# Kernel tuning notes

Measured on AMD Instinct MI355X. Metric: run time of the kernel, lower is better.

The kernel has to match this reference:

```python
import jax, jax.numpy as jnp
import numpy as np

BLOCKSIZE = 64
# Fixed NF4 codebook (bitsandbytes normal-float 4-bit quantiles)
NF4_CODE = jnp.array([
    -1.0, -0.6961928009986877, -0.5250730514526367, -0.39491748809814453,
    -0.28444138169288635, -0.18477343022823334, -0.09105003625154495, 0.0,
    0.07958029955625534, 0.16093020141124725, 0.24611230194568634,
    0.33791524171829224, 0.44070982933044434, 0.5626170039176941,
    0.7229568362236023, 1.0], dtype=jnp.float32)


def setup_inputs() -> dict:
    key = jax.random.key(0)
    k1, k2, k3, k4 = jax.random.split(key, 4)
    B, IN, OUT = 32, 4096, 14336
    x = jax.random.normal(k1, (B, IN), dtype=jnp.float32)
    codes = jax.random.randint(k2, (OUT, IN), 0, 16, dtype=jnp.int32)
    absmax = jax.random.uniform(k3, (OUT * IN // BLOCKSIZE,), dtype=jnp.float32)
    bias = jax.random.normal(k4, (OUT,), dtype=jnp.float32)
    return {"x": x, "codes": codes, "absmax": absmax, "bias": bias}


def reference(x, codes, absmax, bias):
    out_f, in_f = codes.shape
    # Dequantize: codebook lookup then per-block (64) absmax scaling
    w = NF4_CODE[codes].reshape(-1, BLOCKSIZE) * absmax[:, None]  # [nblocks, 64]
    w = w.reshape(out_f, in_f)
    # y = x @ W^T + bias  (matmul_4bit semantics)
    return jnp.einsum('bi,oi->bo', x, w) + bias
```

## Files before the change

kernel.cpp:

```cpp
#include <hip/hip_runtime.h>
#include <stddef.h>
#include <stdint.h>

#define B_     32
#define IN_    4096
#define OUT_   14336
#define KSPLIT 8
#define KRANGE (IN_ / KSPLIT)
#define NSTEP  (KRANGE / 32)
#define POUT   (B_ * OUT_)

typedef _Float16 v2h __attribute__((ext_vector_type(2)));
typedef _Float16 v8h __attribute__((ext_vector_type(8)));
typedef float    v4f __attribute__((ext_vector_type(4)));
typedef int      v4i __attribute__((ext_vector_type(4)));

__device__ __constant__ float c_nf4[16] = {
    -1.0f, -0.6961928009986877f, -0.5250730514526367f, -0.39491748809814453f,
    -0.28444138169288635f, -0.18477343022823334f, -0.09105003625154495f, 0.0f,
    0.07958029955625534f, 0.16093020141124725f, 0.24611230194568634f,
    0.33791524171829224f, 0.44070982933044434f, 0.5626170039176941f,
    0.7229568362236023f, 1.0f};

__global__ __launch_bounds__(256) void prep(const float* __restrict__ x,
                                            unsigned* __restrict__ xB) {
    int t  = blockIdx.x * 256 + threadIdx.x;
    int kt = t >> 7;
    int bt = (t >> 6) & 1;
    int l  = t & 63;
    int b  = bt * 16 + (l & 15);
    int k0 = kt * 32 + (l >> 4) * 8;
    const float* xr = x + (size_t)b * IN_ + k0;
    float4 a = *(const float4*)xr;
    float4 c = *(const float4*)(xr + 4);
    union { v2h h; unsigned u; } p0, p1, p2, p3;
    p0.h = (v2h){(_Float16)a.x, (_Float16)a.y};
    p1.h = (v2h){(_Float16)a.z, (_Float16)a.w};
    p2.h = (v2h){(_Float16)c.x, (_Float16)c.y};
    p3.h = (v2h){(_Float16)c.z, (_Float16)c.w};
    uint4 w = {p0.u, p1.u, p2.u, p3.u};
    *(uint4*)(xB + (size_t)t * 4) = w;
}

__global__ __launch_bounds__(256) void init_out(const float* __restrict__ bias,
                                                float* __restrict__ out) {
    int i4 = (blockIdx.x * 256 + threadIdx.x) * 4;
    int o = i4 % OUT_;
    *(float4*)(out + i4) = *(const float4*)(bias + o);
}

__global__ __launch_bounds__(256) void reduce_out(const float* __restrict__ partial,
                                                  const float* __restrict__ bias,
                                                  float* __restrict__ out) {
    int i4 = (blockIdx.x * 256 + threadIdx.x) * 4;
    int o = i4 % OUT_;
    float4 r = *(const float4*)(bias + o);
#pragma unroll
    for (int s = 0; s < KSPLIT; ++s) {
        float4 p = *(const float4*)(partial + (size_t)s * POUT + i4);
        r.x += p.x; r.y += p.y; r.z += p.z; r.w += p.w;
    }
    *(float4*)(out + i4) = r;
}

#define ROWSTRIDE 67

template <int ATOMIC>
__global__ __launch_bounds__(256) void nf4_mfma(
    const int* __restrict__ codes, const float* __restrict__ absmax,
    const unsigned* __restrict__ xB, float* __restrict__ dst) {
    __shared__ unsigned stage[4 * 16 * ROWSTRIDE];
    __shared__ v2h lut2[256];

    const int tid = threadIdx.x;
    {
        float lo = c_nf4[tid & 15], hi = c_nf4[tid >> 4];
        lut2[tid] = (v2h){(_Float16)lo, (_Float16)hi};
    }
    __syncthreads();

    const int w  = tid >> 6;
    const int l  = tid & 63;
    const int ot = blockIdx.x >> 3;
    const int ks = blockIdx.x & 7;
    const int m  = l & 15;
    const int q  = l >> 4;
    const int o0 = ot * 64 + w * 16;

    unsigned* sw = stage + w * 16 * ROWSTRIDE;

#pragma unroll 4
    for (int i = 0; i < 16; ++i) {
        const v4i* rp = (const v4i*)(codes + (size_t)(o0 + i) * IN_ + ks * KRANGE);
        v4i a0 = __builtin_nontemporal_load(rp + 2 * l);
        v4i a1 = __builtin_nontemporal_load(rp + 2 * l + 1);
        unsigned pk = (unsigned)(a0[0] | (a0[1] << 4)) |
                      ((unsigned)(a0[2] | (a0[3] << 4)) << 8) |
                      ((unsigned)(a1[0] | (a1[1] << 4)) << 16) |
                      ((unsigned)(a1[2] | (a1[3] << 4)) << 24);
        sw[i * ROWSTRIDE + l] = pk;
    }

    const float* amrow = absmax + (size_t)(o0 + m) * 64 + ks * (KRANGE / 64);
    const uint4* xbp   = (const uint4*)xB + (size_t)(ks * NSTEP) * 128 + l;

    v4f acc0 = {0.f, 0.f, 0.f, 0.f};
    v4f acc1 = {0.f, 0.f, 0.f, 0.f};

#pragma unroll 4
    for (int kt = 0; kt < NSTEP; ++kt) {
        unsigned pk = sw[m * ROWSTRIDE + kt * 4 + q];
        uint4 b0 = xbp[(size_t)kt * 128];
        uint4 b1 = xbp[(size_t)kt * 128 + 64];
        float amf = amrow[kt >> 1];
        _Float16 ah = (_Float16)amf;
        v2h amh = (v2h){ah, ah};

        union { v2h h[4]; v8h v; } A;
        A.h[0] = lut2[pk & 255] * amh;
        A.h[1] = lut2[(pk >> 8) & 255] * amh;
        A.h[2] = lut2[(pk >> 16) & 255] * amh;
        A.h[3] = lut2[pk >> 24] * amh;

        union { uint4 u; v8h v; } F0, F1;
        F0.u = b0;
        F1.u = b1;
        acc0 = __builtin_amdgcn_mfma_f32_16x16x32_f16(A.v, F0.v, acc0, 0, 0, 0);
        acc1 = __builtin_amdgcn_mfma_f32_16x16x32_f16(A.v, F1.v, acc1, 0, 0, 0);
    }

    const int bc = l & 15;
    const int ob = o0 + q * 4;
#pragma unroll
    for (int r = 0; r < 4; ++r) {
        if (ATOMIC) {
            atomicAdd(dst + (size_t)bc * OUT_ + ob + r, acc0[r]);
            atomicAdd(dst + (size_t)(bc + 16) * OUT_ + ob + r, acc1[r]);
        } else {
            dst[((size_t)ks * B_ + bc) * OUT_ + ob + r]      = acc0[r];
            dst[((size_t)ks * B_ + bc + 16) * OUT_ + ob + r] = acc1[r];
        }
    }
}

extern "C" void kernel_launch(void* const* d_in, const int* in_sizes, int n_in,
                              void* d_out, int out_size, void* d_ws, size_t ws_size,
                              hipStream_t stream) {
    const float* x      = (const float*)d_in[0];
    const int*   codes  = (const int*)d_in[1];
    const float* absmax = (const float*)d_in[2];
    const float* bias   = (const float*)d_in[3];
    float* out = (float*)d_out;
    unsigned* xB = (unsigned*)d_ws;

    prep<<<dim3(64), 256, 0, stream>>>(x, xB);

    const size_t need = 262144 + (size_t)KSPLIT * POUT * 4;
    if (ws_size >= need) {
        float* partial = (float*)((char*)d_ws + 262144);
        nf4_mfma<0><<<dim3(224 * KSPLIT), 256, 0, stream>>>(codes, absmax, xB, partial);
        reduce_out<<<dim3(POUT / 1024), 256, 0, stream>>>(partial, bias, out);
    } else {
        init_out<<<dim3(POUT / 1024), 256, 0, stream>>>(bias, out);
        nf4_mfma<1><<<dim3(224 * KSPLIT), 256, 0, stream>>>(codes, absmax, xB, out);
    }
}
```

Before: 330.6 us.

## Drop split-K and fuse bias into single-pass NF4 MFMA kernel

Removes the K-split across blocks, so each block now loops over all eight K sections for its 64 output rows. Bias is added in the kernel epilogue, which eliminates the partial-sum buffer, the reduce kernel and the atomic fallback path. Code loads for each section are fully unrolled, and absmax values are fetched as vectors. The grid shrinks from 1792 to 224 blocks, which is fewer than the CU count. That cuts parallelism and latency hiding for a kernel dominated by streaming the int32 codes.

```diff
diff --git a/kernel.cpp b/kernel.cpp
--- a/kernel.cpp
+++ b/kernel.cpp
@@ -2,13 +2,12 @@
 #include <stddef.h>
 #include <stdint.h>
 
-#define B_     32
-#define IN_    4096
-#define OUT_   14336
-#define KSPLIT 8
-#define KRANGE (IN_ / KSPLIT)
-#define NSTEP  (KRANGE / 32)
-#define POUT   (B_ * OUT_)
+#define B_   32
+#define IN_  4096
+#define OUT_ 14336
+#define NSEC 8
+#define SECK 512
+#define ROWSTRIDE 67
 
 typedef _Float16 v2h __attribute__((ext_vector_type(2)));
 typedef _Float16 v8h __attribute__((ext_vector_type(8)));
@@ -42,33 +41,10 @@
     *(uint4*)(xB + (size_t)t * 4) = w;
 }
 
-__global__ __launch_bounds__(256) void init_out(const float* __restrict__ bias,
-                                                float* __restrict__ out) {
-    int i4 = (blockIdx.x * 256 + threadIdx.x) * 4;
-    int o = i4 % OUT_;
-    *(float4*)(out + i4) = *(const float4*)(bias + o);
-}
-
-__global__ __launch_bounds__(256) void reduce_out(const float* __restrict__ partial,
-                                                  const float* __restrict__ bias,
-                                                  float* __restrict__ out) {
-    int i4 = (blockIdx.x * 256 + threadIdx.x) * 4;
-    int o = i4 % OUT_;
-    float4 r = *(const float4*)(bias + o);
-#pragma unroll
-    for (int s = 0; s < KSPLIT; ++s) {
-        float4 p = *(const float4*)(partial + (size_t)s * POUT + i4);
-        r.x += p.x; r.y += p.y; r.z += p.z; r.w += p.w;
-    }
-    *(float4*)(out + i4) = r;
-}
-
-#define ROWSTRIDE 67
-
-template <int ATOMIC>
 __global__ __launch_bounds__(256) void nf4_mfma(
     const int* __restrict__ codes, const float* __restrict__ absmax,
-    const unsigned* __restrict__ xB, float* __restrict__ dst) {
+    const unsigned* __restrict__ xB, const float* __restrict__ bias,
+    float* __restrict__ out) {
     __shared__ unsigned stage[4 * 16 * ROWSTRIDE];
     __shared__ v2h lut2[256];
 
@@ -81,65 +57,65 @@
 
     const int w  = tid >> 6;
     const int l  = tid & 63;
-    const int ot = blockIdx.x >> 3;
-    const int ks = blockIdx.x & 7;
     const int m  = l & 15;
     const int q  = l >> 4;
-    const int o0 = ot * 64 + w * 16;
+    const int o0 = blockIdx.x * 64 + w * 16;
 
     unsigned* sw = stage + w * 16 * ROWSTRIDE;
-
-#pragma unroll 4
-    for (int i = 0; i < 16; ++i) {
-        const v4i* rp = (const v4i*)(codes + (size_t)(o0 + i) * IN_ + ks * KRANGE);
-        v4i a0 = __builtin_nontemporal_load(rp + 2 * l);
-        v4i a1 = __builtin_nontemporal_load(rp + 2 * l + 1);
-        unsigned pk = (unsigned)(a0[0] | (a0[1] << 4)) |
-                      ((unsigned)(a0[2] | (a0[3] << 4)) << 8) |
-                      ((unsigned)(a1[0] | (a1[1] << 4)) << 16) |
-                      ((unsigned)(a1[2] | (a1[3] << 4)) << 24);
-        sw[i * ROWSTRIDE + l] = pk;
-    }
-
-    const float* amrow = absmax + (size_t)(o0 + m) * 64 + ks * (KRANGE / 64);
-    const uint4* xbp   = (const uint4*)xB + (size_t)(ks * NSTEP) * 128 + l;
+    const float* amrow = absmax + (size_t)(o0 + m) * 64;
+    const uint4* xbp   = (const uint4*)xB + l;
 
     v4f acc0 = {0.f, 0.f, 0.f, 0.f};
     v4f acc1 = {0.f, 0.f, 0.f, 0.f};
 
-#pragma unroll 4
-    for (int kt = 0; kt < NSTEP; ++kt) {
-        unsigned pk = sw[m * ROWSTRIDE + kt * 4 + q];
-        uint4 b0 = xbp[(size_t)kt * 128];
-        uint4 b1 = xbp[(size_t)kt * 128 + 64];
-        float amf = amrow[kt >> 1];
-        _Float16 ah = (_Float16)amf;
-        v2h amh = (v2h){ah, ah};
+#pragma unroll 1
+    for (int s = 0; s < NSEC; ++s) {
+#pragma unroll
+        for (int i = 0; i < 16; ++i) {
+            const v4i* rp = (const v4i*)(codes + (size_t)(o0 + i) * IN_ + s * SECK);
+            v4i a0 = __builtin_nontemporal_load(rp + 2 * l);
+            v4i a1 = __builtin_nontemporal_load(rp + 2 * l + 1);
+            unsigned pk = (unsigned)(a0[0] | (a0[1] << 4)) |
+                          ((unsigned)(a0[2] | (a0[3] << 4)) << 8) |
+                          ((unsigned)(a1[0] | (a1[1] << 4)) << 16) |
+                          ((unsigned)(a1[2] | (a1[3] << 4)) << 24);
+            sw[i * ROWSTRIDE + l] = pk;
+        }
 
-        union { v2h h[4]; v8h v; } A;
-        A.h[0] = lut2[pk & 255] * amh;
-        A.h[1] = lut2[(pk >> 8) & 255] * amh;
-        A.h[2] = lut2[(pk >> 16) & 255] * amh;
-        A.h[3] = lut2[pk >> 24] * amh;
+        float4 amlo = *(const float4*)(amrow + s * 8);
+        float4 amhi = *(const float4*)(amrow + s * 8 + 4);
+        const float ams[8] = {amlo.x, amlo.y, amlo.z, amlo.w,
+                              amhi.x, amhi.y, amhi.z, amhi.w};
 
-        union { uint4 u; v8h v; } F0, F1;
-        F0.u = b0;
-        F1.u = b1;
-        acc0 = __builtin_amdgcn_mfma_f32_16x16x32_f16(A.v, F0.v, acc0, 0, 0, 0);
-        acc1 = __builtin_amdgcn_mfma_f32_16x16x32_f16(A.v, F1.v, acc1, 0, 0, 0);
+#pragma unroll
+        for (int kt = 0; kt < 16; ++kt) {
+            unsigned pk = sw[m * ROWSTRIDE + kt * 4 + q];
+            uint4 b0 = xbp[(size_t)(s * 16 + kt) * 128];
+            uint4 b1 = xbp[(size_t)(s * 16 + kt) * 128 + 64];
+            _Float16 ah = (_Float16)ams[kt >> 1];
+            v2h amh = (v2h){ah, ah};
+
+            union { v2h h[4]; v8h v; } A;
+            A.h[0] = lut2[pk & 255] * amh;
+            A.h[1] = lut2[(pk >> 8) & 255] * amh;
+            A.h[2] = lut2[(pk >> 16) & 255] * amh;
+            A.h[3] = lut2[pk >> 24] * amh;
+
+            union { uint4 u; v8h v; } F0, F1;
+            F0.u = b0;
+            F1.u = b1;
+            acc0 = __builtin_amdgcn_mfma_f32_16x16x32_f16(A.v, F0.v, acc0, 0, 0, 0);
+            acc1 = __builtin_amdgcn_mfma_f32_16x16x32_f16(A.v, F1.v, acc1, 0, 0, 0);
+        }
     }
 
     const int bc = l & 15;
     const int ob = o0 + q * 4;
 #pragma unroll
     for (int r = 0; r < 4; ++r) {
-        if (ATOMIC) {
-            atomicAdd(dst + (size_t)bc * OUT_ + ob + r, acc0[r]);
-            atomicAdd(dst + (size_t)(bc + 16) * OUT_ + ob + r, acc1[r]);
-        } else {
-            dst[((size_t)ks * B_ + bc) * OUT_ + ob + r]      = acc0[r];
-            dst[((size_t)ks * B_ + bc + 16) * OUT_ + ob + r] = acc1[r];
-        }
+        float bv = bias[ob + r];
+        out[(size_t)bc * OUT_ + ob + r]        = acc0[r] + bv;
+        out[(size_t)(bc + 16) * OUT_ + ob + r] = acc1[r] + bv;
     }
 }
 
@@ -154,14 +130,5 @@
     unsigned* xB = (unsigned*)d_ws;
 
     prep<<<dim3(64), 256, 0, stream>>>(x, xB);
-
-    const size_t need = 262144 + (size_t)KSPLIT * POUT * 4;
-    if (ws_size >= need) {
-        float* partial = (float*)((char*)d_ws + 262144);
-        nf4_mfma<0><<<dim3(224 * KSPLIT), 256, 0, stream>>>(codes, absmax, xB, partial);
-        reduce_out<<<dim3(POUT / 1024), 256, 0, stream>>>(partial, bias, out);
-    } else {
-        init_out<<<dim3(POUT / 1024), 256, 0, stream>>>(bias, out);
-        nf4_mfma<1><<<dim3(224 * KSPLIT), 256, 0, stream>>>(codes, absmax, xB, out);
-    }
+    nf4_mfma<<<dim3(OUT_ / 64), 256, 0, stream>>>(codes, absmax, xB, bias, out);
 }
```

Result: slower. 366.8 us (+10.9%).
